# Optimization experiments

Measured on AMD Instinct MI355X. Metric: run time of the kernel, lower is better.

Reference implementation:

```python
import jax, jax.numpy as jnp
import numpy as np

NUM_ELMT = 64
INPUT_DIM = 16
BOUND = 50.0
MESH_RATIO = 1.2
N_POINTS = 1_048_576


def _build_mesh():
    m = NUM_ELMT
    one_step = BOUND * (MESH_RATIO - 1.0) / (MESH_RATIO ** (m / 2) - 1.0)
    idx = np.arange(-m / 2, m / 2 + 1)
    mesh = (MESH_RATIO ** np.abs(idx) - 1.0) / (MESH_RATIO - 1.0) * one_step * np.sign(idx)
    mesh_norm = (mesh + BOUND) / (2.0 * BOUND)
    mesh_norm = np.concatenate([[0.0], mesh_norm[1:-1], [1.0]]).astype(np.float32)
    elmt_size = (mesh_norm[1:] - mesh_norm[:-1]).astype(np.float32)
    return jnp.asarray(mesh_norm), jnp.asarray(elmt_size)


def setup_inputs() -> dict:
    key = jax.random.key(0)
    k1, k2 = jax.random.split(key)
    x = jax.random.uniform(k1, (N_POINTS, INPUT_DIM), jnp.float32, minval=-BOUND, maxval=BOUND)
    pdj = jnp.ones((N_POINTS, 1), jnp.float32)
    sldj = jnp.zeros((N_POINTS, 1), jnp.float32)
    log_p = 0.1 * jax.random.normal(k2, (NUM_ELMT - 1, INPUT_DIM), jnp.float32)
    mesh_norm, elmt_size = _build_mesh()
    return {"x": x, "pdj": pdj, "sldj": sldj, "log_p": log_p,
            "mesh_norm": mesh_norm, "elmt_size": elmt_size}


def _normalize_pdf(log_p, elmt_size):
    # elmt_size: (M,) -> (M,1) column, log_p: (M-1, D)
    es = elmt_size[:, None]
    ep = jnp.exp(log_p)
    px = ep * (es[:-1] + es[1:]) / 2.0
    px = ep * (1.0 - es[0]) / jnp.sum(px, axis=0, keepdims=True)
    p0 = jnp.ones((1, log_p.shape[1]), log_p.dtype)
    pdf_norm = jnp.concatenate([p0, px, p0], axis=0)            # (M+1, D)
    cell = (pdf_norm[:-1] + pdf_norm[1:]) / 2.0 * es            # (M, D)
    # F_ref[i] = sum(cell[:i]); single cumsum instead of the O(M^2) torch loop
    F_ref = jnp.concatenate([jnp.zeros_like(p0), jnp.cumsum(cell, axis=0)[:-1]], axis=0)  # (M, D)
    return pdf_norm, F_ref


def reference(x, pdj, sldj, log_p, mesh_norm, elmt_size):
    pdf_norm, F_ref = _normalize_pdf(log_p, elmt_size)
    xn = (x + BOUND) / (2.0 * BOUND)                            # (N, D) in [0,1]
    k = jnp.searchsorted(mesh_norm, xn, side='left')            # (N, D), torch right=False
    cover = (k != 0) & (k != NUM_ELMT + 1)
    k = jnp.clip(k, 1, NUM_ELMT)
    km1 = k - 1
    v1 = jnp.take_along_axis(pdf_norm, km1, axis=0)             # pdf at lower node
    v2 = jnp.take_along_axis(pdf_norm, k, axis=0)               # pdf at upper node
    xmodi = xn - mesh_norm[km1]                                 # offset inside element
    h = elmt_size[km1]                                          # element width
    F_pre = jnp.take_along_axis(F_ref, km1, axis=0)             # CDF at lower node
    y = jnp.where(cover, F_pre + xmodi * xmodi * 0.5 * (v2 - v1) / h + xmodi * v1, xn)
    abs_det = jnp.where(cover, xmodi * (v2 - v1) / h + v1, 1.0)
    pdj_out = pdj * jnp.prod(abs_det, axis=-1, keepdims=True)
    sldj_out = sldj + jnp.sum(jnp.log(abs_det), axis=-1, keepdims=True)
    x_out = y * 2.0 * BOUND - BOUND
    return (x_out, pdj_out, sldj_out)
```

## Files before the change

kernel.cpp:

```cpp
#include <hip/hip_runtime.h>
#include <math.h>
#include <stdint.h>


namespace {
constexpr int DIM = 16;
constexpr int ME  = 64;
constexpr float BOUNDF = 50.0f;
constexpr float K1      = 6.8164378f;
constexpr float INV_L2R = 3.8017840f;
constexpr int NBIN = 66;
constexpr int ROWF = 68;
constexpr int TABLE_FLOATS = NBIN * ROWF;
}

__global__ __launch_bounds__(256) void nll_setup(
    const float* __restrict__ log_p,
    const float* __restrict__ mesh_norm,
    float* __restrict__ table)
{
  __shared__ float s_mesh[ME + 1];
  const int tid = threadIdx.x;
  if (tid <= ME) s_mesh[tid] = mesh_norm[tid];
  __syncthreads();

  const int wv = tid >> 6, lane = tid & 63;
  const float mj  = s_mesh[lane];
  const float mj1 = s_mesh[lane + 1];
  const float mj2 = s_mesh[(lane + 2 > ME) ? ME : (lane + 2)];
  const float es0 = s_mesh[1] - s_mesh[0];
  const float h = mj1 - mj;

#pragma unroll
  for (int i = 0; i < 4; ++i) {
    const int d = 4 * wv + i;
    const float ep = (lane < 63) ? __expf(log_p[lane * DIM + d]) : 0.f;
    float ss = (lane < 63) ? ep * (mj2 - mj) : 0.f;
    ss += __shfl_xor(ss, 1);  ss += __shfl_xor(ss, 2);  ss += __shfl_xor(ss, 4);
    ss += __shfl_xor(ss, 8);  ss += __shfl_xor(ss, 16); ss += __shfl_xor(ss, 32);
    const float scale = (1.0f - es0) / (0.5f * ss);
    const float cur = (lane < 63) ? ep * scale : 1.0f;
    float prev = __shfl_up(cur, 1);
    if (lane == 0) prev = 1.0f;
    const float cell = (prev + cur) * 0.5f * h;
    float v = cell, o;
    o = __shfl_up(v, 1);  if (lane >= 1)  v += o;
    o = __shfl_up(v, 2);  if (lane >= 2)  v += o;
    o = __shfl_up(v, 4);  if (lane >= 4)  v += o;
    o = __shfl_up(v, 8);  if (lane >= 8)  v += o;
    o = __shfl_up(v, 16); if (lane >= 16) v += o;
    o = __shfl_up(v, 32); if (lane >= 32) v += o;
    const float F = v - cell;
    const float A = 0.5f * (cur - prev) / h;
    const float B = fmaf(-(A + A), mj, prev);
    const float D = fmaf(mj, fmaf(mj, A, -prev), F);
    *reinterpret_cast<float4*>(&table[(lane + 1) * ROWF + 4 * d]) =
        make_float4(A, B, D, A + A);
  }
  if (tid < 32) {
    const int row = (tid >> 4) ? (NBIN - 1) : 0;
    const int d = tid & 15;
    *reinterpret_cast<float4*>(&table[row * ROWF + 4 * d]) =
        make_float4(0.f, 1.f, 0.f, 0.f);
  }
}

__global__ __launch_bounds__(256) void nll_main(
    const float* __restrict__ x,
    const float* __restrict__ pdj,
    const float* __restrict__ sldj,
    const float* __restrict__ table,
    float* __restrict__ out,
    int npts, int npairs)
{
  __shared__ __align__(16) float co[TABLE_FLOATS];

  const int tid = threadIdx.x;
  {
    const float4* t4 = reinterpret_cast<const float4*>(table);
    float4* c4 = reinterpret_cast<float4*>(co);
#pragma unroll
    for (int i = 0; i < 5; ++i) {
      const int idx = tid + 256 * i;
      if (idx < TABLE_FLOATS / 4) c4[idx] = t4[idx];
    }
  }
  __syncthreads();

  const int t = blockIdx.x * blockDim.x + tid;
  if (t >= npairs) return;

  const float4* __restrict__ x4 = reinterpret_cast<const float4*>(x);
  float4* __restrict__ out4 = reinterpret_cast<float4*>(out);
  const int np16 = npts * DIM;

  const int p  = t >> 1;
  const int hh = t & 1;
  const int dbase = hh << 5;
  const float4 xa = x4[2 * t];
  const float4 xb = x4[2 * t + 1];
  const float ps = hh ? sldj[p] : pdj[p];
  const float vals[8] = {xa.x, xa.y, xa.z, xa.w, xb.x, xb.y, xb.z, xb.w};

  float xn[8];
  int   idx[8];
#pragma unroll
  for (int j = 0; j < 8; ++j) {
    const float val = vals[j];
    xn[j] = fmaf(val, 0.01f, 0.5f);
    const float u = fmaf(fabsf(val), K1, 1.0f);
    const float n = __log2f(u) * INV_L2R;
    int k = 32 + (int)ceilf(copysignf(n, val));
    k = k < 0 ? 0 : (k > NBIN - 1 ? NBIN - 1 : k);
    idx[j] = k * ROWF + dbase + (j << 2);
  }

  float4 cf[8];
#pragma unroll
  for (int j = 0; j < 8; ++j)
    cf[j] = *reinterpret_cast<const float4*>(&co[idx[j]]);

  float yv[8], dt[8];
#pragma unroll
  for (int j = 0; j < 8; ++j) {
    const float z = xn[j];
    yv[j] = fmaf(fmaf(z, fmaf(z, cf[j].x, cf[j].y), cf[j].z), 2.0f * BOUNDF, -BOUNDF);
    dt[j] = fmaf(z, cf[j].w, cf[j].y);
  }
  const float prod = ((dt[0] * dt[1]) * (dt[2] * dt[3])) *
                     ((dt[4] * dt[5]) * (dt[6] * dt[7]));

  out4[2 * t]     = make_float4(yv[0], yv[1], yv[2], yv[3]);
  out4[2 * t + 1] = make_float4(yv[4], yv[5], yv[6], yv[7]);

  const float full = prod * __shfl_xor(prod, 1);
  const float res  = hh ? (ps + __logf(full)) : (ps * full);
  out[np16 + hh * npts + p] = res;
}

extern "C" void kernel_launch(void* const* d_in, const int* in_sizes, int n_in,
                              void* d_out, int out_size, void* d_ws, size_t ws_size,
                              hipStream_t stream) {
  const float* x    = (const float*)d_in[0];
  const float* pdj  = (const float*)d_in[1];
  const float* sldj = (const float*)d_in[2];
  const float* lp   = (const float*)d_in[3];
  const float* mesh = (const float*)d_in[4];
  float* out   = (float*)d_out;
  float* table = (float*)d_ws;

  const int npts   = in_sizes[0] / DIM;
  const int npairs = npts * 2;
  const int block  = 256;
  const int grid   = (npairs + block - 1) / block;

  hipLaunchKernelGGL(nll_setup, dim3(1), dim3(block), 0, stream, lp, mesh, table);
  hipLaunchKernelGGL(nll_main, dim3(grid), dim3(block), 0, stream,
                     x, pdj, sldj, table, out, npts, npairs);
}
```

Baseline: 35.85 us.

## Fuse table setup into main kernel, recomputing coefficients per block

Removes the single-block setup kernel and the global table round trip. Each 512-thread block now rebuilds the coefficient table in shared memory from log_p and mesh_norm, and issues its x/pdj/sldj loads before that work so the global loads overlap it. This drops one launch and the serial dependency between the two kernels. In exchange every block repeats the exp, shuffle reductions and scans, and the larger block size changes occupancy.

```diff
diff --git a/kernel.cpp b/kernel.cpp
--- a/kernel.cpp
+++ b/kernel.cpp
@@ -11,95 +11,85 @@
 constexpr float INV_L2R = 3.8017840f;
 constexpr int NBIN = 66;
 constexpr int ROWF = 68;
-constexpr int TABLE_FLOATS = NBIN * ROWF;
+constexpr int COEF_FLOATS = NBIN * ROWF;
+constexpr int BLOCK = 512;
 }
 
-__global__ __launch_bounds__(256) void nll_setup(
-    const float* __restrict__ log_p,
-    const float* __restrict__ mesh_norm,
-    float* __restrict__ table)
-{
-  __shared__ float s_mesh[ME + 1];
-  const int tid = threadIdx.x;
-  if (tid <= ME) s_mesh[tid] = mesh_norm[tid];
-  __syncthreads();
-
-  const int wv = tid >> 6, lane = tid & 63;
-  const float mj  = s_mesh[lane];
-  const float mj1 = s_mesh[lane + 1];
-  const float mj2 = s_mesh[(lane + 2 > ME) ? ME : (lane + 2)];
-  const float es0 = s_mesh[1] - s_mesh[0];
-  const float h = mj1 - mj;
-
-#pragma unroll
-  for (int i = 0; i < 4; ++i) {
-    const int d = 4 * wv + i;
-    const float ep = (lane < 63) ? __expf(log_p[lane * DIM + d]) : 0.f;
-    float ss = (lane < 63) ? ep * (mj2 - mj) : 0.f;
-    ss += __shfl_xor(ss, 1);  ss += __shfl_xor(ss, 2);  ss += __shfl_xor(ss, 4);
-    ss += __shfl_xor(ss, 8);  ss += __shfl_xor(ss, 16); ss += __shfl_xor(ss, 32);
-    const float scale = (1.0f - es0) / (0.5f * ss);
-    const float cur = (lane < 63) ? ep * scale : 1.0f;
-    float prev = __shfl_up(cur, 1);
-    if (lane == 0) prev = 1.0f;
-    const float cell = (prev + cur) * 0.5f * h;
-    float v = cell, o;
-    o = __shfl_up(v, 1);  if (lane >= 1)  v += o;
-    o = __shfl_up(v, 2);  if (lane >= 2)  v += o;
-    o = __shfl_up(v, 4);  if (lane >= 4)  v += o;
-    o = __shfl_up(v, 8);  if (lane >= 8)  v += o;
-    o = __shfl_up(v, 16); if (lane >= 16) v += o;
-    o = __shfl_up(v, 32); if (lane >= 32) v += o;
-    const float F = v - cell;
-    const float A = 0.5f * (cur - prev) / h;
-    const float B = fmaf(-(A + A), mj, prev);
-    const float D = fmaf(mj, fmaf(mj, A, -prev), F);
-    *reinterpret_cast<float4*>(&table[(lane + 1) * ROWF + 4 * d]) =
-        make_float4(A, B, D, A + A);
-  }
-  if (tid < 32) {
-    const int row = (tid >> 4) ? (NBIN - 1) : 0;
-    const int d = tid & 15;
-    *reinterpret_cast<float4*>(&table[row * ROWF + 4 * d]) =
-        make_float4(0.f, 1.f, 0.f, 0.f);
-  }
-}
-
-__global__ __launch_bounds__(256) void nll_main(
+__global__ __launch_bounds__(BLOCK) void nll_kernel(
     const float* __restrict__ x,
     const float* __restrict__ pdj,
     const float* __restrict__ sldj,
-    const float* __restrict__ table,
+    const float* __restrict__ log_p,
+    const float* __restrict__ mesh_norm,
     float* __restrict__ out,
     int npts, int npairs)
 {
-  __shared__ __align__(16) float co[TABLE_FLOATS];
+  __shared__ __align__(16) float co[COEF_FLOATS];
 
-  const int tid = threadIdx.x;
+  const int tid  = threadIdx.x;
+  const int wv   = tid >> 6;
+  const int lane = tid & 63;
+
+  const int t = blockIdx.x * BLOCK + tid;
+  const bool live = t < npairs;
+
+  const float4* __restrict__ x4 = reinterpret_cast<const float4*>(x);
+  float4 xa, xb;
+  float ps = 0.f;
+  if (live) {
+    xa = x4[2 * t];
+    xb = x4[2 * t + 1];
+    ps = (t & 1) ? sldj[t >> 1] : pdj[t >> 1];
+  }
+
   {
-    const float4* t4 = reinterpret_cast<const float4*>(table);
-    float4* c4 = reinterpret_cast<float4*>(co);
+    const float mj  = mesh_norm[lane];
+    const float mj1 = mesh_norm[lane + 1];
+    const float mj2 = mesh_norm[(lane + 2 > ME) ? ME : (lane + 2)];
+    const float es0 = mesh_norm[1];
+    const float h = mj1 - mj;
 #pragma unroll
-    for (int i = 0; i < 5; ++i) {
-      const int idx = tid + 256 * i;
-      if (idx < TABLE_FLOATS / 4) c4[idx] = t4[idx];
+    for (int i = 0; i < 2; ++i) {
+      const int d = 2 * wv + i;
+      const float ep = (lane < 63) ? __expf(log_p[lane * DIM + d]) : 0.f;
+      float ss = (lane < 63) ? ep * (mj2 - mj) : 0.f;
+      ss += __shfl_xor(ss, 1);  ss += __shfl_xor(ss, 2);  ss += __shfl_xor(ss, 4);
+      ss += __shfl_xor(ss, 8);  ss += __shfl_xor(ss, 16); ss += __shfl_xor(ss, 32);
+      const float scale = (1.0f - es0) / (0.5f * ss);
+      const float cur = (lane < 63) ? ep * scale : 1.0f;
+      float prev = __shfl_up(cur, 1);
+      if (lane == 0) prev = 1.0f;
+      const float cell = (prev + cur) * 0.5f * h;
+      float v = cell, o;
+      o = __shfl_up(v, 1);  if (lane >= 1)  v += o;
+      o = __shfl_up(v, 2);  if (lane >= 2)  v += o;
+      o = __shfl_up(v, 4);  if (lane >= 4)  v += o;
+      o = __shfl_up(v, 8);  if (lane >= 8)  v += o;
+      o = __shfl_up(v, 16); if (lane >= 16) v += o;
+      o = __shfl_up(v, 32); if (lane >= 32) v += o;
+      const float F = v - cell;
+      const float A = 0.5f * (cur - prev) / h;
+      const float B = fmaf(-(A + A), mj, prev);
+      const float D = fmaf(mj, fmaf(mj, A, -prev), F);
+      *reinterpret_cast<float4*>(&co[(lane + 1) * ROWF + 4 * d]) =
+          make_float4(A, B, D, A + A);
+    }
+    if (tid < 32) {
+      const int row = (tid >> 4) ? (NBIN - 1) : 0;
+      const int d = tid & 15;
+      *reinterpret_cast<float4*>(&co[row * ROWF + 4 * d]) =
+          make_float4(0.f, 1.f, 0.f, 0.f);
     }
   }
   __syncthreads();
 
-  const int t = blockIdx.x * blockDim.x + tid;
-  if (t >= npairs) return;
+  if (!live) return;
 
-  const float4* __restrict__ x4 = reinterpret_cast<const float4*>(x);
   float4* __restrict__ out4 = reinterpret_cast<float4*>(out);
   const int np16 = npts * DIM;
-
   const int p  = t >> 1;
   const int hh = t & 1;
   const int dbase = hh << 5;
-  const float4 xa = x4[2 * t];
-  const float4 xb = x4[2 * t + 1];
-  const float ps = hh ? sldj[p] : pdj[p];
   const float vals[8] = {xa.x, xa.y, xa.z, xa.w, xb.x, xb.y, xb.z, xb.w};
 
   float xn[8];
@@ -146,15 +136,12 @@
   const float* sldj = (const float*)d_in[2];
   const float* lp   = (const float*)d_in[3];
   const float* mesh = (const float*)d_in[4];
-  float* out   = (float*)d_out;
-  float* table = (float*)d_ws;
+  float* out = (float*)d_out;
 
   const int npts   = in_sizes[0] / DIM;
   const int npairs = npts * 2;
-  const int block  = 256;
-  const int grid   = (npairs + block - 1) / block;
+  const int grid   = (npairs + BLOCK - 1) / BLOCK;
 
-  hipLaunchKernelGGL(nll_setup, dim3(1), dim3(block), 0, stream, lp, mesh, table);
-  hipLaunchKernelGGL(nll_main, dim3(grid), dim3(block), 0, stream,
-                     x, pdj, sldj, table, out, npts, npairs);
+  hipLaunchKernelGGL(nll_kernel, dim3(grid), dim3(BLOCK), 0, stream,
+                     x, pdj, sldj, lp, mesh, out, npts, npairs);
 }
```

New measurement: 32.53 us, median of 2. 9.3% less time.
